# Performance work log

Measured on AMD Instinct MI355X. Metric: run time of the kernel, lower is better.

The kernel has to match this reference:

```python
import jax, jax.numpy as jnp
import numpy as np

N_NODES = 25000
N_EDGES = 250000
DIM = 64
HEADS = 4
BN_EPS = 1e-5


def setup_inputs() -> dict:
    key = jax.random.key(0)
    ks = jax.random.split(key, 6)
    x = jax.random.normal(ks[0], (N_NODES, DIM), dtype=jnp.float32)
    edge_index = jax.random.randint(ks[1], (2, N_EDGES), 0, N_NODES)
    edge_attr = jax.random.normal(ks[2], (N_EDGES, DIM), dtype=jnp.float32)
    # learned params of GATGNN_AGAT_LAYER (xavier-ish scale)
    W = jax.random.normal(ks[3], (2 * DIM, HEADS * DIM), dtype=jnp.float32) * 0.05
    att = jax.random.normal(ks[4], (1, HEADS, 2 * DIM), dtype=jnp.float32) * 0.05
    bias = jnp.zeros((DIM,), dtype=jnp.float32)
    # BatchNorm1d(heads) in eval mode (running stats)
    bn_gamma = jnp.ones((HEADS,), dtype=jnp.float32)
    bn_beta = jnp.zeros((HEADS,), dtype=jnp.float32)
    bn_mean = jnp.zeros((HEADS,), dtype=jnp.float32)
    bn_var = jnp.ones((HEADS,), dtype=jnp.float32)
    return {"x": x, "edge_attr": edge_attr, "W": W, "att": att, "bias": bias,
            "bn_gamma": bn_gamma, "bn_beta": bn_beta, "bn_mean": bn_mean,
            "bn_var": bn_var, "edge_index": edge_index}


def reference(x, edge_attr, W, att, bias, bn_gamma, bn_beta, bn_mean, bn_var, edge_index):
    act = jax.nn.softplus  # act='softplus' in DSDCrystal
    # flow='target_to_source': i = edge_index[0] (aggregation index), j = edge_index[1]
    idx_i = edge_index[0]
    idx_j = edge_index[1]
    x_i = x[idx_i]                                   # [E, D] gather
    x_j = x[idx_j]                                   # [E, D] gather
    out_i = act(jnp.concatenate([x_i, edge_attr], axis=-1) @ W)  # [E, H*D]
    out_j = act(jnp.concatenate([x_j, edge_attr], axis=-1) @ W)  # [E, H*D]
    out_i = out_i.reshape(-1, HEADS, DIM)            # [E, H, D]
    out_j = out_j.reshape(-1, HEADS, DIM)
    # multi-head attention logits
    alpha = act(jnp.sum(jnp.concatenate([out_i, out_j], axis=-1) * att, axis=-1))  # [E, H]
    # BatchNorm1d(heads), eval mode
    alpha = act((alpha - bn_mean) / jnp.sqrt(bn_var + BN_EPS) * bn_gamma + bn_beta)
    # segment softmax over edges sharing the same target node i
    amax = jax.ops.segment_max(alpha, idx_i, num_segments=N_NODES)  # [N, H]
    e = jnp.exp(alpha - amax[idx_i])
    denom = jax.ops.segment_sum(e, idx_i, num_segments=N_NODES)[idx_i]  # [E, H]
    alpha = e / denom
    # weighted messages, scatter-add aggregation (dropout p=0.0 / eval)
    msg = out_j * alpha[:, :, None]                  # [E, H, D]
    aggr = jax.ops.segment_sum(msg, idx_i, num_segments=N_NODES)  # [N, H, D]
    # update: mean over heads + bias
    return aggr.mean(axis=1) + bias                  # [N, D]
```

## Files before the change

### kernel.cpp

```cpp
#include <hip/hip_runtime.h>
#include <hip/hip_bf16.h>
#include <math.h>

#define NN 25000
#define NE 250000
#define DD 64
#define HH 4
#define NGROUP (NE / 16)

typedef __attribute__((ext_vector_type(8))) short bf16x8;
typedef __attribute__((ext_vector_type(4))) float f32x4;

#define WT_LD 136

__device__ __forceinline__ float softplus_f(float x) {
    return fmaxf(x, 0.0f) + __logf(1.0f + __expf(-fabsf(x)));
}

__device__ __forceinline__ unsigned short f2bf(float f) {
    __hip_bfloat16 h = __float2bfloat16(f);
    unsigned short u;
    __builtin_memcpy(&u, &h, 2);
    return u;
}

__device__ __forceinline__ float bf2f(unsigned short u) {
    return __uint_as_float(((unsigned int)u) << 16);
}

__device__ __forceinline__ void load8(const float* p, bf16x8& hi, bf16x8& lo) {
    float4 a = *(const float4*)p;
    float4 b = *(const float4*)(p + 4);
    float v[8] = {a.x, a.y, a.z, a.w, b.x, b.y, b.z, b.w};
#pragma unroll
    for (int i = 0; i < 8; ++i) {
        unsigned short h = f2bf(v[i]);
        hi[i] = (short)h;
        lo[i] = (short)f2bf(v[i] - bf2f(h));
    }
}

__global__ __launch_bounds__(512, 4)
void k_edge(const float* __restrict__ x, const float* __restrict__ ea,
            const float* __restrict__ W, const float* __restrict__ att,
            const float* __restrict__ bn_g, const float* __restrict__ bn_b,
            const float* __restrict__ bn_m, const float* __restrict__ bn_v,
            const int* __restrict__ eidx,
            unsigned short* __restrict__ outj,
            float* __restrict__ expa, float* __restrict__ denom)
{
    __shared__ unsigned short Wsh[256 * WT_LD];
    __shared__ float attI[256], attJ[256];

    const int tid = threadIdx.x;
    const int lane = tid & 63;
    const int q = lane >> 4;
    const int r = lane & 15;

    for (int idx = tid; idx < 32768; idx += 512) {
        int k = idx >> 8, n = idx & 255;
        Wsh[n * WT_LD + k] = f2bf(W[idx]);
    }
    if (tid < 256) {
        int c = tid;
        attI[c] = att[(c >> 6) * 128 + (c & 63)];
        attJ[c] = att[(c >> 6) * 128 + 64 + (c & 63)];
    }
    float bnsc[HH], bnsh[HH];
#pragma unroll
    for (int t = 0; t < HH; ++t) {
        float inv = rsqrtf(bn_v[t] + 1e-5f);
        bnsc[t] = bn_g[t] * inv;
        bnsh[t] = bn_b[t] - bn_m[t] * bn_g[t] * inv;
    }
    __syncthreads();

    const int gw = blockIdx.x * 8 + (tid >> 6);
    const int nw = gridDim.x * 8;

    for (int g = gw; g < NGROUP; g += nw) {
        const int e0 = g * 16;
        const int ei = eidx[e0 + r];
        const int ej = eidx[NE + e0 + r];
        const float* xi = x + (size_t)ei * DD;
        const float* xj = x + (size_t)ej * DD;
        const float* ev = ea + (size_t)(e0 + r) * DD;

        bf16x8 Ahi[6], Alo[6];
        load8(xi + q * 8,      Ahi[0], Alo[0]);
        load8(xi + 32 + q * 8, Ahi[1], Alo[1]);
        load8(xj + q * 8,      Ahi[2], Alo[2]);
        load8(xj + 32 + q * 8, Ahi[3], Alo[3]);
        load8(ev + q * 8,      Ahi[4], Alo[4]);
        load8(ev + 32 + q * 8, Ahi[5], Alo[5]);

        float lg[4][4];
#pragma unroll
        for (int a = 0; a < 4; ++a)
#pragma unroll
            for (int b = 0; b < 4; ++b) lg[a][b] = 0.f;

#pragma unroll
        for (int nt = 0; nt < 4; ++nt) {
            f32x4 ai[4], aj[4];
#pragma unroll
            for (int h = 0; h < 4; ++h) {
                ai[h] = (f32x4){0.f, 0.f, 0.f, 0.f};
                aj[h] = (f32x4){0.f, 0.f, 0.f, 0.f};
            }
#pragma unroll
            for (int h = 0; h < 4; ++h) {
                const unsigned short* bp = &Wsh[((nt + 4 * h) * 16 + r) * WT_LD + q * 8];
#pragma unroll
                for (int kt = 0; kt < 4; ++kt) {
                    bf16x8 bf = *(const bf16x8*)(bp + kt * 32);
                    const int fi = (kt < 2) ? kt : kt + 2;
                    const int fj = kt + 2;
                    ai[h] = __builtin_amdgcn_mfma_f32_16x16x32_bf16(Ahi[fi], bf, ai[h], 0, 0, 0);
                    ai[h] = __builtin_amdgcn_mfma_f32_16x16x32_bf16(Alo[fi], bf, ai[h], 0, 0, 0);
                    aj[h] = __builtin_amdgcn_mfma_f32_16x16x32_bf16(Ahi[fj], bf, aj[h], 0, 0, 0);
                    aj[h] = __builtin_amdgcn_mfma_f32_16x16x32_bf16(Alo[fj], bf, aj[h], 0, 0, 0);
                }
            }
            const int dbase = nt * 16 + r;
#pragma unroll
            for (int reg = 0; reg < 4; ++reg) {
                ushort4 pk;
                unsigned short* pkp = (unsigned short*)&pk;
#pragma unroll
                for (int h = 0; h < 4; ++h) {
                    const int c = dbase + 64 * h;
                    float spi = softplus_f(ai[h][reg]);
                    float spj = softplus_f(aj[h][reg]);
                    lg[reg][h] += spi * attI[c] + spj * attJ[c];
                    pkp[h] = f2bf(spj);
                }
                const unsigned e = (unsigned)(e0 + q * 4 + reg);
                *(ushort4*)&outj[e * 256 + dbase * 4] = pk;
            }
        }

#pragma unroll
        for (int off = 1; off < 16; off <<= 1) {
#pragma unroll
            for (int a = 0; a < 4; ++a)
#pragma unroll
                for (int b = 0; b < 4; ++b)
                    lg[a][b] += __shfl_xor(lg[a][b], off, 64);
        }
        float exv[4][4];
#pragma unroll
        for (int reg = 0; reg < 4; ++reg)
#pragma unroll
            for (int h = 0; h < 4; ++h)
                exv[reg][h] = __expf(softplus_f(fmaf(lg[reg][h], bnsc[h], bnsh[h])));

        if (r < 4) {
#pragma unroll
            for (int reg = 0; reg < 4; ++reg) {
                const int e = e0 + q * 4 + reg;
                const int ii = eidx[e];
                expa[e * 4 + r] = exv[reg][r];
                atomicAdd(&denom[ii * 4 + r], exv[reg][r]);
            }
        }
    }
}

__global__ __launch_bounds__(256)
void k_scatter(const int* __restrict__ eidx,
               const unsigned short* __restrict__ outj,
               const float* __restrict__ expa,
               const float* __restrict__ denom,
               float* __restrict__ acc)
{
    const int e = blockIdx.x * 4 + (threadIdx.x >> 6);
    const int lane = threadIdx.x & 63;
    const int i = eidx[e];
    float4 ev = *(const float4*)&expa[e * 4];
    float4 dv = *(const float4*)&denom[i * 4];
    float w0 = 0.25f * ev.x / dv.x;
    float w1 = 0.25f * ev.y / dv.y;
    float w2 = 0.25f * ev.z / dv.z;
    float w3 = 0.25f * ev.w / dv.w;
    ushort4 v = *(const ushort4*)&outj[((unsigned)e << 8) | (lane << 2)];
    float s = w0 * bf2f(v.x) + w1 * bf2f(v.y) + w2 * bf2f(v.z) + w3 * bf2f(v.w);
    atomicAdd(&acc[i * DD + lane], s);
}

__global__ __launch_bounds__(256)
void k_final(const float* __restrict__ acc, const float* __restrict__ bias,
             float* __restrict__ out)
{
    const int t = blockIdx.x * 256 + threadIdx.x;
    out[t] = acc[t] + bias[t & 63];
}

extern "C" void kernel_launch(void* const* d_in, const int* in_sizes, int n_in,
                              void* d_out, int out_size, void* d_ws, size_t ws_size,
                              hipStream_t stream)
{
    (void)in_sizes; (void)n_in; (void)out_size; (void)ws_size;
    const float* x    = (const float*)d_in[0];
    const float* ea   = (const float*)d_in[1];
    const float* W    = (const float*)d_in[2];
    const float* att  = (const float*)d_in[3];
    const float* bias = (const float*)d_in[4];
    const float* bn_g = (const float*)d_in[5];
    const float* bn_b = (const float*)d_in[6];
    const float* bn_m = (const float*)d_in[7];
    const float* bn_v = (const float*)d_in[8];
    const int*   eidx = (const int*)d_in[9];
    float* out = (float*)d_out;

    char* ws = (char*)d_ws;
    unsigned short* outj = (unsigned short*)ws;
    float* expa  = (float*)(ws + (size_t)NE * 256 * 2);
    float* denom = (float*)(ws + (size_t)NE * 256 * 2 + (size_t)NE * 16);
    float* acc   = denom + (size_t)NN * 4;

    hipMemsetAsync(denom, 0, (size_t)(NN * 4 + NN * DD) * sizeof(float), stream);

    k_edge<<<dim3(512), dim3(512), 0, stream>>>(
        x, ea, W, att, bn_g, bn_b, bn_m, bn_v, eidx, outj, expa, denom);
    k_scatter<<<dim3(NE / 4), dim3(256), 0, stream>>>(eidx, outj, expa, denom, acc);
    k_final<<<dim3((NN * DD) / 256), dim3(256), 0, stream>>>(acc, bias, out);
}
```

Baseline: 306.2 us.

## Replace atomic scatter with CSR-sorted per-node gather aggregation

Builds a CSR edge list grouped by target node (histogram, single-block scan, fill) and replaces the atomic denominator and message scatter with a per-node gather kernel. That kernel computes the softmax denominator and the weighted sum in registers and writes the output directly, removing the float atomics and the final bias kernel. The edge kernel is also reshaped to 1024-thread blocks with half as many blocks. The cost is three extra small launches, including a serial single-block scan, plus random reads of outj per node.

```diff
diff --git a/kernel.cpp b/kernel.cpp
--- a/kernel.cpp
+++ b/kernel.cpp
@@ -40,14 +40,14 @@
     }
 }
 
-__global__ __launch_bounds__(512, 4)
+__global__ __launch_bounds__(1024, 2)
 void k_edge(const float* __restrict__ x, const float* __restrict__ ea,
             const float* __restrict__ W, const float* __restrict__ att,
             const float* __restrict__ bn_g, const float* __restrict__ bn_b,
             const float* __restrict__ bn_m, const float* __restrict__ bn_v,
             const int* __restrict__ eidx,
             unsigned short* __restrict__ outj,
-            float* __restrict__ expa, float* __restrict__ denom)
+            float* __restrict__ expa)
 {
     __shared__ unsigned short Wsh[256 * WT_LD];
     __shared__ float attI[256], attJ[256];
@@ -57,7 +57,7 @@
     const int q = lane >> 4;
     const int r = lane & 15;
 
-    for (int idx = tid; idx < 32768; idx += 512) {
+    for (int idx = tid; idx < 32768; idx += 1024) {
         int k = idx >> 8, n = idx & 255;
         Wsh[n * WT_LD + k] = f2bf(W[idx]);
     }
@@ -75,8 +75,8 @@
     }
     __syncthreads();
 
-    const int gw = blockIdx.x * 8 + (tid >> 6);
-    const int nw = gridDim.x * 8;
+    const int gw = blockIdx.x * 16 + (tid >> 6);
+    const int nw = gridDim.x * 16;
 
     for (int g = gw; g < NGROUP; g += nw) {
         const int e0 = g * 16;
@@ -159,41 +159,100 @@
 #pragma unroll
             for (int reg = 0; reg < 4; ++reg) {
                 const int e = e0 + q * 4 + reg;
-                const int ii = eidx[e];
                 expa[e * 4 + r] = exv[reg][r];
-                atomicAdd(&denom[ii * 4 + r], exv[reg][r]);
             }
         }
     }
 }
 
 __global__ __launch_bounds__(256)
-void k_scatter(const int* __restrict__ eidx,
-               const unsigned short* __restrict__ outj,
-               const float* __restrict__ expa,
-               const float* __restrict__ denom,
-               float* __restrict__ acc)
-{
-    const int e = blockIdx.x * 4 + (threadIdx.x >> 6);
+void k_hist(const int* __restrict__ eidx, int* __restrict__ deg)
+{
+    const int e = blockIdx.x * 256 + threadIdx.x;
+    if (e < NE) atomicAdd(&deg[eidx[e]], 1);
+}
+
+__global__ __launch_bounds__(1024)
+void k_scan(const int* __restrict__ deg, int* __restrict__ offs)
+{
+    __shared__ int sh[1024];
+    const int t = threadIdx.x;
+    const int base = t * 25;
+    int s = 0;
+#pragma unroll
+    for (int k = 0; k < 25; ++k) {
+        int idx = base + k;
+        if (idx < NN) s += deg[idx];
+    }
+    sh[t] = s;
+    __syncthreads();
+    for (int off = 1; off < 1024; off <<= 1) {
+        int v = (t >= off) ? sh[t - off] : 0;
+        __syncthreads();
+        sh[t] += v;
+        __syncthreads();
+    }
+    int run = sh[t] - s;
+#pragma unroll
+    for (int k = 0; k < 25; ++k) {
+        int idx = base + k;
+        if (idx < NN) {
+            offs[idx] = run;
+            run += deg[idx];
+        } else if (idx == NN) {
+            offs[NN] = run;
+        }
+    }
+}
+
+__global__ __launch_bounds__(256)
+void k_fill(const int* __restrict__ eidx, const int* __restrict__ offs,
+            int* __restrict__ cursor, int* __restrict__ elist)
+{
+    const int e = blockIdx.x * 256 + threadIdx.x;
+    if (e < NE) {
+        const int i = eidx[e];
+        const int p = atomicAdd(&cursor[i], 1);
+        elist[offs[i] + p] = e;
+    }
+}
+
+__global__ __launch_bounds__(256)
+void k_aggr(const int* __restrict__ offs, const int* __restrict__ elist,
+            const unsigned short* __restrict__ outj,
+            const float* __restrict__ expa,
+            const float* __restrict__ bias, float* __restrict__ out)
+{
+    const int n = blockIdx.x * 4 + (threadIdx.x >> 6);
     const int lane = threadIdx.x & 63;
-    const int i = eidx[e];
-    float4 ev = *(const float4*)&expa[e * 4];
-    float4 dv = *(const float4*)&denom[i * 4];
-    float w0 = 0.25f * ev.x / dv.x;
-    float w1 = 0.25f * ev.y / dv.y;
-    float w2 = 0.25f * ev.z / dv.z;
-    float w3 = 0.25f * ev.w / dv.w;
-    ushort4 v = *(const ushort4*)&outj[((unsigned)e << 8) | (lane << 2)];
-    float s = w0 * bf2f(v.x) + w1 * bf2f(v.y) + w2 * bf2f(v.z) + w3 * bf2f(v.w);
-    atomicAdd(&acc[i * DD + lane], s);
-}
-
-__global__ __launch_bounds__(256)
-void k_final(const float* __restrict__ acc, const float* __restrict__ bias,
-             float* __restrict__ out)
-{
-    const int t = blockIdx.x * 256 + threadIdx.x;
-    out[t] = acc[t] + bias[t & 63];
+    const int beg = offs[n];
+    const int end = offs[n + 1];
+
+    float4 s = make_float4(0.f, 0.f, 0.f, 0.f);
+    for (int t = beg + lane; t < end; t += 64) {
+        const int e = elist[t];
+        float4 v = *(const float4*)&expa[e * 4];
+        s.x += v.x; s.y += v.y; s.z += v.z; s.w += v.w;
+    }
+#pragma unroll
+    for (int off = 32; off >= 1; off >>= 1) {
+        s.x += __shfl_xor(s.x, off, 64);
+        s.y += __shfl_xor(s.y, off, 64);
+        s.z += __shfl_xor(s.z, off, 64);
+        s.w += __shfl_xor(s.w, off, 64);
+    }
+    const float w0 = 0.25f / s.x, w1 = 0.25f / s.y;
+    const float w2 = 0.25f / s.z, w3 = 0.25f / s.w;
+
+    float sum = 0.f;
+    for (int t = beg; t < end; ++t) {
+        const int e = elist[t];
+        float4 ev = *(const float4*)&expa[e * 4];
+        ushort4 v = *(const ushort4*)&outj[((unsigned)e << 8) | (lane << 2)];
+        sum += (ev.x * w0) * bf2f(v.x) + (ev.y * w1) * bf2f(v.y)
+             + (ev.z * w2) * bf2f(v.z) + (ev.w * w3) * bf2f(v.w);
+    }
+    out[n * DD + lane] = sum + bias[lane];
 }
 
 extern "C" void kernel_launch(void* const* d_in, const int* in_sizes, int n_in,
@@ -215,14 +274,18 @@
 
     char* ws = (char*)d_ws;
     unsigned short* outj = (unsigned short*)ws;
-    float* expa  = (float*)(ws + (size_t)NE * 256 * 2);
-    float* denom = (float*)(ws + (size_t)NE * 256 * 2 + (size_t)NE * 16);
-    float* acc   = denom + (size_t)NN * 4;
-
-    hipMemsetAsync(denom, 0, (size_t)(NN * 4 + NN * DD) * sizeof(float), stream);
-
-    k_edge<<<dim3(512), dim3(512), 0, stream>>>(
-        x, ea, W, att, bn_g, bn_b, bn_m, bn_v, eidx, outj, expa, denom);
-    k_scatter<<<dim3(NE / 4), dim3(256), 0, stream>>>(eidx, outj, expa, denom, acc);
-    k_final<<<dim3((NN * DD) / 256), dim3(256), 0, stream>>>(acc, bias, out);
-}
+    float* expa  = (float*)(ws + 128000000ull);
+    int*   deg    = (int*)(ws + 132000000ull);
+    int*   cursor = (int*)(ws + 132100000ull);
+    int*   offs   = (int*)(ws + 132200000ull);
+    int*   elist  = (int*)(ws + 132300032ull);
+
+    hipMemsetAsync(deg, 0, 200000, stream);
+
+    k_hist<<<dim3((NE + 255) / 256), dim3(256), 0, stream>>>(eidx, deg);
+    k_scan<<<dim3(1), dim3(1024), 0, stream>>>(deg, offs);
+    k_fill<<<dim3((NE + 255) / 256), dim3(256), 0, stream>>>(eidx, offs, cursor, elist);
+    k_edge<<<dim3(256), dim3(1024), 0, stream>>>(
+        x, ea, W, att, bn_g, bn_b, bn_m, bn_v, eidx, outj, expa);
+    k_aggr<<<dim3(NN / 4), dim3(256), 0, stream>>>(offs, elist, outj, expa, bias, out);
+}
```

After: 356.7 us. +16.5%, slower.
